# Kernel optimization log

Measured on AMD Instinct MI355X. Metric: run time of the kernel, lower is better.

Reference implementation:

```python
import jax, jax.numpy as jnp
import numpy as np

B = 512       # batch_size
IN = 256      # input_size
H = 512       # hidden_size
OUT = 64      # output_size
N_PAIRS = B - 1   # number of H0 persistence deaths (connected components merges)
TOL = 1e-6    # rtol for torch.isclose
ATOL = 1e-8   # torch default atol
EPS = 0.0     # homology_eps
TARGET_P = 1.0
HOM_P = 1.0
COMP_P = 0.01

_IU = np.triu_indices(B, 1)  # condensed pdist indexing, static


def _mlp(batch, W1, b1, W2, b2, W3, b3, Wout, bout):
    # FeedForward: input->hidden, (n_layers-1) hidden->hidden, hidden->output, ReLU
    h = jax.nn.relu(batch @ W1 + b1)
    h = jax.nn.relu(h @ W2 + b2)
    h = jax.nn.relu(h @ W3 + b3)
    return h @ Wout + bout


def _pdist(y):
    # condensed euclidean pairwise distances, same ordering as torch F.pdist
    d = y[_IU[0]] - y[_IU[1]]                 # [P, OUT]
    return jnp.sqrt(jnp.sum(d * d, axis=-1))  # [P]


def setup_inputs() -> dict:
    key = jax.random.key(0)
    ks = jax.random.split(key, 8)
    batch = jax.random.normal(ks[0], (B, IN), jnp.float32)
    target = jax.random.normal(ks[1], (B, OUT), jnp.float32)
    W1 = jax.random.normal(ks[2], (IN, H), jnp.float32) / np.sqrt(IN)
    W2 = jax.random.normal(ks[3], (H, H), jnp.float32) / np.sqrt(H)
    W3 = jax.random.normal(ks[4], (H, H), jnp.float32) / np.sqrt(H)
    Wout = jax.random.normal(ks[5], (H, OUT), jnp.float32) / np.sqrt(H)
    b1 = jnp.zeros((H,), jnp.float32)
    b2 = jnp.zeros((H,), jnp.float32)
    b3 = jnp.zeros((H,), jnp.float32)
    bout = jnp.zeros((OUT,), jnp.float32)
    # persistence deaths = actual critical pdist values (from the external
    # Vietoris-Rips routine in the original); sample N_PAIRS distinct entries.
    y0 = _mlp(batch, W1, b1, W2, b2, W3, b3, Wout, bout)
    pd0 = np.asarray(_pdist(y0))
    idx = np.random.default_rng(0).choice(pd0.shape[0], N_PAIRS, replace=False)
    persistence_deaths = jnp.asarray(pd0[idx], jnp.float32)
    return {"batch": batch, "target": target,
            "W1": W1, "b1": b1, "W2": W2, "b2": b2, "W3": W3, "b3": b3,
            "Wout": Wout, "bout": bout,
            "persistence_deaths": persistence_deaths}


def reference(batch, target, W1, b1, W2, b2, W3, b3, Wout, bout, persistence_deaths):
    y = _mlp(batch, W1, b1, W2, b2, W3, b3, Wout, bout)   # [B, OUT]
    y_hom = y  # normalize_for_homology = False
    pd = _pdist(y_hom)                                     # [P]
    # vectorized indicator_death over all pairs (replaces per-pair Python loop)
    mask = jnp.any(jnp.isclose(pd[:, None], persistence_deaths[None, :],
                               rtol=TOL, atol=ATOL), axis=1)      # [P] bool
    # homology_dim=0: birth_pdist = 0; norm=1 of selected (death - 0 + eps)
    homology_loss = jnp.sum(jnp.abs(jnp.where(mask, pd + EPS, 0.0)))
    target_loss = jnp.mean((target - y) ** 2)
    compactness_loss = jnp.sum(jnp.abs(y - jnp.mean(y, axis=0, keepdims=True)))
    loss = TARGET_P * target_loss + HOM_P * homology_loss + COMP_P * compactness_loss
    return loss
```

## Files before the change

kernel.cpp:

```cpp
#include <hip/hip_runtime.h>

#define B_    512
#define IN_   256
#define H_    512
#define OUT_  64
#define NDEATH (B_ - 1)
#define NSORT  512
#define RTOL_ 1e-6
#define ATOL_ 1e-8
#define NBLK  256
#define NTHR  512
#define KT    32

typedef __attribute__((ext_vector_type(4))) double d4_t;

__device__ __forceinline__ void ast(double* p, double v) {
    __hip_atomic_store(p, v, __ATOMIC_RELAXED, __HIP_MEMORY_SCOPE_AGENT);
}
__device__ __forceinline__ double ald(const double* p) {
    return __hip_atomic_load(p, __ATOMIC_RELAXED, __HIP_MEMORY_SCOPE_AGENT);
}
__device__ __forceinline__ unsigned aldu(const unsigned* p) {
    return __hip_atomic_load(p, __ATOMIC_RELAXED, __HIP_MEMORY_SCOPE_AGENT);
}
__device__ __forceinline__ void aadd(unsigned* p) {
    __hip_atomic_fetch_add(p, 1u, __ATOMIC_RELAXED, __HIP_MEMORY_SCOPE_AGENT);
}

__device__ __forceinline__ void lbar() {
    asm volatile("s_waitcnt lgkmcnt(0)" ::: "memory");
    __builtin_amdgcn_s_barrier();
    asm volatile("" ::: "memory");
}

__device__ __forceinline__ void gbar(unsigned* cnt, unsigned nb) {
    __syncthreads();
    if (threadIdx.x == 0) {
        aadd(cnt);
        while (aldu(cnt) < nb) __builtin_amdgcn_s_sleep(1);
    }
    __syncthreads();
}

__device__ __forceinline__ void gbar2(unsigned* gslot, unsigned* root,
                                      int leader) {
    __syncthreads();
    if (threadIdx.x == 0) {
        aadd(gslot);
        if (leader) {
            while (aldu(gslot) < 16u) __builtin_amdgcn_s_sleep(1);
            aadd(root);
        }
        while (aldu(root) < 16u) __builtin_amdgcn_s_sleep(1);
    }
    __syncthreads();
}

__device__ void sort_windows(const float* __restrict__ deaths,
                             double* sd, double* slo, double* shi, int t) {
    if (t < NSORT) sd[t] = (t < NDEATH) ? (double)deaths[t] : 1e300;
    __syncthreads();
    for (int k = 2; k <= NSORT; k <<= 1) {
        for (int j = k >> 1; j > 0; j >>= 1) {
            if (t < 256) {
                int l = ((t & ~(j - 1)) << 1) | (t & (j - 1));
                int p = l + j;
                bool up = ((l & k) == 0);
                double a = sd[l], b = sd[p];
                if ((a > b) == up) { sd[l] = b; sd[p] = a; }
            }
            __syncthreads();
        }
    }
    if (t < NSORT) {
        double d = sd[t];
        double w = ATOL_ + RTOL_ * fabs(d);
        slo[t] = d - w;
        shi[t] = d + w;
    }
    __syncthreads();
}

template <typename TIN, bool RELU, int N, int K>
__device__ void gemm_dev(const TIN* __restrict__ A, const float* __restrict__ W,
                         const float* __restrict__ bias, double* __restrict__ C,
                         int tile, int t,
                         double (&As)[2][2][KT][33]) {
    const int lane  = t & 63;
    const int wave4 = (t >> 6) & 3;
    const int w2    = t >> 8;
    const int tg    = t & 255;
    const int wm    = wave4 & 1, wn = wave4 >> 1;
    constexpr int nbx = N >> 5;
    const int row0  = (tile / nbx) << 5;
    const int col0  = (tile % nbx) << 5;

    const int akk   = tg & 31;
    const int amm   = tg >> 5;
    const int kbase = w2 * (K >> 1);
    constexpr int nkt = K >> 6;

    const int mrow  = wm * 16 + (lane & 15);
    const int ncol  = wn * 16 + (lane & 15);
    const int kq    = lane >> 4;

    TIN   ar[3][4];
    float br[3][8];

    auto load_a = [&](int rs, int kt) {
        const int k0 = kbase + (kt << 5);
        #pragma unroll
        for (int p = 0; p < 4; ++p)
            ar[rs][p] = A[(size_t)(row0 + amm + 8 * p) * K + k0 + akk];
    };
    auto load_b = [&](int rs, int kt) {
        const int k0 = kbase + (kt << 5);
        const float* wp = W + (size_t)(k0 + kq) * N + col0 + ncol;
        #pragma unroll
        for (int ks = 0; ks < 8; ++ks)
            br[rs][ks] = wp[(size_t)(4 * ks) * N];
    };
    auto stage_a = [&](int rs, int buf) {
        #pragma unroll
        for (int p = 0; p < 4; ++p)
            As[w2][buf][akk][amm + 8 * p] = (double)ar[rs][p];
    };

    load_a(0, 0); load_b(0, 0);
    if (nkt > 1) { load_a(1, 1); load_b(1, 1); }
    if (nkt > 2) { load_a(2, 2); load_b(2, 2); }
    stage_a(0, 0);
    lbar();

    d4_t c4a = {0.0, 0.0, 0.0, 0.0};
    d4_t c4b = {0.0, 0.0, 0.0, 0.0};

    #pragma unroll
    for (int kt = 0; kt < nkt; ++kt) {
        const int cur = kt & 1;
        const int rs  = kt % 3;
        __builtin_amdgcn_s_setprio(1);
        #pragma unroll
        for (int ks = 0; ks < 4; ++ks) {
            double av = As[w2][cur][ks * 4 + kq][mrow];
            c4a = __builtin_amdgcn_mfma_f64_16x16x4f64(av, (double)br[rs][ks],
                                                       c4a, 0, 0, 0);
        }
        #pragma unroll
        for (int ks = 4; ks < 8; ++ks) {
            double av = As[w2][cur][ks * 4 + kq][mrow];
            c4b = __builtin_amdgcn_mfma_f64_16x16x4f64(av, (double)br[rs][ks],
                                                       c4b, 0, 0, 0);
        }
        __builtin_amdgcn_s_setprio(0);
        if (kt + 3 < nkt) { load_a(rs, kt + 3); load_b(rs, kt + 3); }
        if (kt + 1 < nkt) stage_a((kt + 1) % 3, cur ^ 1);
        lbar();
    }

    d4_t c4 = c4a + c4b;

    double (*cEx)[16][17] = (double (*)[16][17])(&As[0][0][0][0]);
    const int r4 = (lane >> 4) * 4;
    if (w2 == 1) {
        #pragma unroll
        for (int r = 0; r < 4; ++r)
            cEx[wave4][r4 + r][lane & 15] = c4[r];
    }
    lbar();
    if (w2 == 0) {
        #pragma unroll
        for (int r = 0; r < 4; ++r) {
            int row = row0 + wm * 16 + r4 + r;
            int col = col0 + wn * 16 + (lane & 15);
            double v = c4[r] + cEx[wave4][r4 + r][lane & 15] + (double)bias[col];
            if (RELU) v = v > 0.0 ? v : 0.0;
            ast(&C[(size_t)row * N + col], v);
        }
    }
}

__device__ void mc_dev(const float* __restrict__ target,
                       const double* __restrict__ y,
                       double* __restrict__ t_part, double* __restrict__ c_part,
                       int c, int t) {
    const int wave = t >> 6, lane = t & 63;
    double v = y[(size_t)t * OUT_ + c];
    double s = v;
    for (int off = 32; off; off >>= 1) s += __shfl_down(s, off);
    __shared__ double swm[8];
    __shared__ double smean;
    if (lane == 0) swm[wave] = s;
    __syncthreads();
    if (t == 0) {
        double m = 0.0;
        #pragma unroll
        for (int w = 0; w < 8; ++w) m += swm[w];
        smean = m / (double)B_;
    }
    __syncthreads();
    double m = smean;
    double d = (double)target[(size_t)t * OUT_ + c] - v;
    double t_s = d * d;
    double c_s = fabs(v - m);
    for (int off = 32; off; off >>= 1) {
        t_s += __shfl_down(t_s, off);
        c_s += __shfl_down(c_s, off);
    }
    __shared__ double st[8], sc[8];
    if (lane == 0) { st[wave] = t_s; sc[wave] = c_s; }
    __syncthreads();
    if (t == 0) {
        double ts = 0.0, cs = 0.0;
        #pragma unroll
        for (int w = 0; w < 8; ++w) { ts += st[w]; cs += sc[w]; }
        ast(&t_part[c], ts);
        ast(&c_part[c], cs);
    }
}

__device__ __forceinline__ double pair_val(const double* __restrict__ yrow_s,
                                           const double* __restrict__ yj,
                                           const double* __restrict__ slo,
                                           const double* __restrict__ shi) {
    double s = 0.0;
    #pragma unroll
    for (int d = 0; d < OUT_; d += 2) {
        double2 v = *(const double2*)(yj + d);
        double d0 = yrow_s[d]     - v.x;
        double d1 = yrow_s[d + 1] - v.y;
        s = fma(d0, d0, s);
        s = fma(d1, d1, s);
    }
    double pd = sqrt(s);
    int pos = 0;
    #pragma unroll
    for (int step = NSORT / 2; step; step >>= 1) {
        if (slo[pos + step - 1] <= pd) pos += step;
    }
    bool m = (pos > 0) && (shi[pos - 1] >= pd);
    return m ? pd : 0.0;
}

__device__ void pdist_dev(const double* __restrict__ y,
                          double* __restrict__ hom_part, int bid, int t,
                          double* yA, double* yB,
                          const double* slo, const double* shi) {
    const int iA = bid;
    const int iB = 510 - bid;
    if (t < OUT_)            yA[t]        = y[(size_t)iA * OUT_ + t];
    else if (t < 2 * OUT_)   yB[t - OUT_] = y[(size_t)iB * OUT_ + (t - OUT_)];
    __syncthreads();

    double local = 0.0;
    for (int j = iA + 1 + t; j < B_; j += NTHR)
        local += pair_val(yA, y + (size_t)j * OUT_, slo, shi);
    if (iB != iA)
        for (int j = iB + 1 + t; j < B_; j += NTHR)
            local += pair_val(yB, y + (size_t)j * OUT_, slo, shi);

    for (int off = 32; off; off >>= 1) local += __shfl_down(local, off);
    __shared__ double sw[8];
    int wave = t >> 6, lane = t & 63;
    if (lane == 0) sw[wave] = local;
    __syncthreads();
    if (t == 0) {
        double s = 0.0;
        #pragma unroll
        for (int w = 0; w < 8; ++w) s += sw[w];
        ast(&hom_part[bid], s);
    }
}

__global__ __launch_bounds__(NTHR) void fused_k(
    const float* __restrict__ batch, const float* __restrict__ target,
    const float* __restrict__ W1, const float* __restrict__ b1,
    const float* __restrict__ W2, const float* __restrict__ b2,
    const float* __restrict__ W3, const float* __restrict__ b3,
    const float* __restrict__ Wout, const float* __restrict__ bout,
    const float* __restrict__ deaths, float* __restrict__ out,
    double* __restrict__ hA, double* __restrict__ hB,
    double* __restrict__ hC, double* __restrict__ yv,
    double* __restrict__ hom_part, double* __restrict__ t_part,
    double* __restrict__ c_part, unsigned* __restrict__ cnt,
    double* __restrict__ wbc) {
    const int bid = blockIdx.x;
    const int t   = threadIdx.x;
    const int g   = (bid & 7) | ((bid >> 7) << 3);
    const int c   = (bid >> 3) & 15;
    const int tile = g * 16 + c;
    unsigned* gc  = cnt + g * 32;

    __shared__ double As[2][2][KT][33];
    __shared__ double slo[NSORT], shi[NSORT];
    __shared__ double yA[OUT_], yB[OUT_];
    double* sd = &As[0][0][0][0];

    gemm_dev<float,  true, H_, IN_>(batch, W1, b1, hA, tile, t, As);
    gbar(&gc[0], 16);
    gemm_dev<double, true, H_, H_>(hA, W2, b2, hB, tile, t, As);
    gbar(&gc[1], 16);
    gemm_dev<double, true, H_, H_>(hB, W3, b3, hC, tile, t, As);
    gbar(&gc[2], 16);

    if (c < 2) {
        gemm_dev<double, false, OUT_, H_>(hC, Wout, bout, yv, g * 2 + c, t, As);
    } else {
        sort_windows(deaths, sd, slo, shi, t);
        if (g == 0 && c == 2 && t < NSORT) {
            ast(&wbc[t],         slo[t]);
            ast(&wbc[NSORT + t], shi[t]);
        }
    }

    gbar2(&gc[3], &cnt[512], c == 0);
    if (c < 2) {
        if (t < NSORT) {
            slo[t] = ald(&wbc[t]);
            shi[t] = ald(&wbc[NSORT + t]);
        }
        __syncthreads();
    }

    pdist_dev(yv, hom_part, bid, t, yA, yB, slo, shi);
    if (bid < OUT_) mc_dev(target, yv, t_part, c_part, bid, t);

    __syncthreads();
    if (t == 0) {
        aadd(&gc[4]);
        if (c == 0) {
            while (aldu(&gc[4]) < 16u) __builtin_amdgcn_s_sleep(1);
            aadd(&cnt[513]);
        }
    }
    if (bid != 0) return;
    if (t == 0)
        while (aldu(&cnt[513]) < 16u) __builtin_amdgcn_s_sleep(1);
    __syncthreads();

    {
        double h = 0.0, tp = 0.0, cp = 0.0;
        if (t < NBLK) h = ald(&hom_part[t]);
        if (t < OUT_) { tp = ald(&t_part[t]); cp = ald(&c_part[t]); }
        for (int off = 32; off; off >>= 1) {
            h  += __shfl_down(h,  off);
            tp += __shfl_down(tp, off);
            cp += __shfl_down(cp, off);
        }
        __shared__ double sh[8], stp[8], scp[8];
        int wave = t >> 6, lane = t & 63;
        if (lane == 0) { sh[wave] = h; stp[wave] = tp; scp[wave] = cp; }
        __syncthreads();
        if (t == 0) {
            double hs = 0.0, ts = 0.0, cs = 0.0;
            #pragma unroll
            for (int w = 0; w < 8; ++w) {
                hs += sh[w]; ts += stp[w]; cs += scp[w];
            }
            out[0] = (float)(ts / (double)(B_ * OUT_) + hs + 0.01 * cs);
        }
    }
}

extern "C" void kernel_launch(void* const* d_in, const int* in_sizes, int n_in,
                              void* d_out, int out_size, void* d_ws, size_t ws_size,
                              hipStream_t stream) {
    const float* batch  = (const float*)d_in[0];
    const float* target = (const float*)d_in[1];
    const float* W1     = (const float*)d_in[2];
    const float* b1     = (const float*)d_in[3];
    const float* W2     = (const float*)d_in[4];
    const float* b2     = (const float*)d_in[5];
    const float* W3     = (const float*)d_in[6];
    const float* b3     = (const float*)d_in[7];
    const float* Wout   = (const float*)d_in[8];
    const float* bout   = (const float*)d_in[9];
    const float* deaths = (const float*)d_in[10];
    float* out = (float*)d_out;

    double* hA       = (double*)d_ws;
    double* hB       = hA + (size_t)B_ * H_;
    double* hC       = hB + (size_t)B_ * H_;
    double* yv       = hC + (size_t)B_ * H_;
    double* hom_part = yv + (size_t)B_ * OUT_;
    double* t_part   = hom_part + NBLK;
    double* c_part   = t_part + OUT_;
    unsigned* cnt    = (unsigned*)(c_part + OUT_);
    double* wbc      = (double*)(cnt + 576);

    hipMemsetAsync(cnt, 0, 576 * sizeof(unsigned), stream);

    fused_k<<<dim3(NBLK), dim3(NTHR), 0, stream>>>(
        batch, target, W1, b1, W2, b2, W3, b3, Wout, bout, deaths, out,
        hA, hB, hC, yv, hom_part, t_part, c_part, cnt, wbc);
}
```

Measured before the change: 123.4 us.

## Split persistent fused kernel into six launches instead of grid barriers

Replaces the single persistent kernel, which used atomic-counter grid barriers, with separate kernel launches for each MLP layer, the output GEMM, pdist plus the loss partials, and the final reduction. The window sort now runs in an extra block of the first GEMM launch. This drops the spin-wait barriers, the counter memset and the atomic loads and stores, but adds launch overhead between stages and loses the overlap of sorting with the output GEMM.

```diff
diff --git a/kernel.cpp b/kernel.cpp
--- a/kernel.cpp
+++ b/kernel.cpp
@@ -8,52 +8,15 @@
 #define NSORT  512
 #define RTOL_ 1e-6
 #define ATOL_ 1e-8
-#define NBLK  256
 #define NTHR  512
 #define KT    32
 
 typedef __attribute__((ext_vector_type(4))) double d4_t;
-
-__device__ __forceinline__ void ast(double* p, double v) {
-    __hip_atomic_store(p, v, __ATOMIC_RELAXED, __HIP_MEMORY_SCOPE_AGENT);
-}
-__device__ __forceinline__ double ald(const double* p) {
-    return __hip_atomic_load(p, __ATOMIC_RELAXED, __HIP_MEMORY_SCOPE_AGENT);
-}
-__device__ __forceinline__ unsigned aldu(const unsigned* p) {
-    return __hip_atomic_load(p, __ATOMIC_RELAXED, __HIP_MEMORY_SCOPE_AGENT);
-}
-__device__ __forceinline__ void aadd(unsigned* p) {
-    __hip_atomic_fetch_add(p, 1u, __ATOMIC_RELAXED, __HIP_MEMORY_SCOPE_AGENT);
-}
 
 __device__ __forceinline__ void lbar() {
     asm volatile("s_waitcnt lgkmcnt(0)" ::: "memory");
     __builtin_amdgcn_s_barrier();
     asm volatile("" ::: "memory");
-}
-
-__device__ __forceinline__ void gbar(unsigned* cnt, unsigned nb) {
-    __syncthreads();
-    if (threadIdx.x == 0) {
-        aadd(cnt);
-        while (aldu(cnt) < nb) __builtin_amdgcn_s_sleep(1);
-    }
-    __syncthreads();
-}
-
-__device__ __forceinline__ void gbar2(unsigned* gslot, unsigned* root,
-                                      int leader) {
-    __syncthreads();
-    if (threadIdx.x == 0) {
-        aadd(gslot);
-        if (leader) {
-            while (aldu(gslot) < 16u) __builtin_amdgcn_s_sleep(1);
-            aadd(root);
-        }
-        while (aldu(root) < 16u) __builtin_amdgcn_s_sleep(1);
-    }
-    __syncthreads();
 }
 
 __device__ void sort_windows(const float* __restrict__ deaths,
@@ -175,48 +138,52 @@
             int col = col0 + wn * 16 + (lane & 15);
             double v = c4[r] + cEx[wave4][r4 + r][lane & 15] + (double)bias[col];
             if (RELU) v = v > 0.0 ? v : 0.0;
-            ast(&C[(size_t)row * N + col], v);
-        }
-    }
-}
-
-__device__ void mc_dev(const float* __restrict__ target,
-                       const double* __restrict__ y,
-                       double* __restrict__ t_part, double* __restrict__ c_part,
-                       int c, int t) {
-    const int wave = t >> 6, lane = t & 63;
-    double v = y[(size_t)t * OUT_ + c];
-    double s = v;
-    for (int off = 32; off; off >>= 1) s += __shfl_down(s, off);
-    __shared__ double swm[8];
-    __shared__ double smean;
-    if (lane == 0) swm[wave] = s;
-    __syncthreads();
-    if (t == 0) {
-        double m = 0.0;
-        #pragma unroll
-        for (int w = 0; w < 8; ++w) m += swm[w];
-        smean = m / (double)B_;
-    }
-    __syncthreads();
-    double m = smean;
-    double d = (double)target[(size_t)t * OUT_ + c] - v;
-    double t_s = d * d;
-    double c_s = fabs(v - m);
-    for (int off = 32; off; off >>= 1) {
-        t_s += __shfl_down(t_s, off);
-        c_s += __shfl_down(c_s, off);
-    }
-    __shared__ double st[8], sc[8];
-    if (lane == 0) { st[wave] = t_s; sc[wave] = c_s; }
-    __syncthreads();
-    if (t == 0) {
-        double ts = 0.0, cs = 0.0;
-        #pragma unroll
-        for (int w = 0; w < 8; ++w) { ts += st[w]; cs += sc[w]; }
-        ast(&t_part[c], ts);
-        ast(&c_part[c], cs);
-    }
+            C[(size_t)row * N + col] = v;
+        }
+    }
+}
+
+__device__ __forceinline__ int tile_map(int bid) {
+    const int g = (bid & 7) | ((bid >> 7) << 3);
+    const int c = (bid >> 3) & 15;
+    return g * 16 + c;
+}
+
+__global__ __launch_bounds__(NTHR) void g1s_k(
+    const float* __restrict__ batch, const float* __restrict__ W1,
+    const float* __restrict__ b1, double* __restrict__ hA,
+    const float* __restrict__ deaths, double* __restrict__ wbc) {
+    __shared__ double As[2][2][KT][33];
+    const int t = threadIdx.x, bid = blockIdx.x;
+    if (bid == 256) {
+        double* sd  = &As[0][0][0][0];
+        double* slo = sd + NSORT;
+        double* shi = sd + 2 * NSORT;
+        sort_windows(deaths, sd, slo, shi, t);
+        if (t < NSORT) {
+            wbc[t]         = slo[t];
+            wbc[NSORT + t] = shi[t];
+        }
+        return;
+    }
+    gemm_dev<float, true, H_, IN_>(batch, W1, b1, hA, tile_map(bid), t, As);
+}
+
+template <bool RELU>
+__global__ __launch_bounds__(NTHR) void gemm_k(
+    const double* __restrict__ A, const float* __restrict__ W,
+    const float* __restrict__ bias, double* __restrict__ C) {
+    __shared__ double As[2][2][KT][33];
+    gemm_dev<double, RELU, H_, H_>(A, W, bias, C, tile_map(blockIdx.x),
+                                   threadIdx.x, As);
+}
+
+__global__ __launch_bounds__(NTHR) void gout_k(
+    const double* __restrict__ hC, const float* __restrict__ Wout,
+    const float* __restrict__ bout, double* __restrict__ yv) {
+    __shared__ double As[2][2][KT][33];
+    gemm_dev<double, false, OUT_, H_>(hC, Wout, bout, yv, blockIdx.x,
+                                      threadIdx.x, As);
 }
 
 __device__ __forceinline__ double pair_val(const double* __restrict__ yrow_s,
@@ -268,97 +235,83 @@
         double s = 0.0;
         #pragma unroll
         for (int w = 0; w < 8; ++w) s += sw[w];
-        ast(&hom_part[bid], s);
-    }
-}
-
-__global__ __launch_bounds__(NTHR) void fused_k(
-    const float* __restrict__ batch, const float* __restrict__ target,
-    const float* __restrict__ W1, const float* __restrict__ b1,
-    const float* __restrict__ W2, const float* __restrict__ b2,
-    const float* __restrict__ W3, const float* __restrict__ b3,
-    const float* __restrict__ Wout, const float* __restrict__ bout,
-    const float* __restrict__ deaths, float* __restrict__ out,
-    double* __restrict__ hA, double* __restrict__ hB,
-    double* __restrict__ hC, double* __restrict__ yv,
-    double* __restrict__ hom_part, double* __restrict__ t_part,
-    double* __restrict__ c_part, unsigned* __restrict__ cnt,
-    double* __restrict__ wbc) {
-    const int bid = blockIdx.x;
-    const int t   = threadIdx.x;
-    const int g   = (bid & 7) | ((bid >> 7) << 3);
-    const int c   = (bid >> 3) & 15;
-    const int tile = g * 16 + c;
-    unsigned* gc  = cnt + g * 32;
-
-    __shared__ double As[2][2][KT][33];
+        hom_part[bid] = s;
+    }
+}
+
+__device__ void mc_dev(const float* __restrict__ target,
+                       const double* __restrict__ y,
+                       double* __restrict__ t_part, double* __restrict__ c_part,
+                       int c, int t) {
+    const int wave = t >> 6, lane = t & 63;
+    double v = y[(size_t)t * OUT_ + c];
+    double s = v;
+    for (int off = 32; off; off >>= 1) s += __shfl_down(s, off);
+    __shared__ double swm[8];
+    __shared__ double smean;
+    if (lane == 0) swm[wave] = s;
+    __syncthreads();
+    if (t == 0) {
+        double m = 0.0;
+        #pragma unroll
+        for (int w = 0; w < 8; ++w) m += swm[w];
+        smean = m / (double)B_;
+    }
+    __syncthreads();
+    double m = smean;
+    double d = (double)target[(size_t)t * OUT_ + c] - v;
+    double t_s = d * d;
+    double c_s = fabs(v - m);
+    for (int off = 32; off; off >>= 1) {
+        t_s += __shfl_down(t_s, off);
+        c_s += __shfl_down(c_s, off);
+    }
+    __shared__ double st[8], sc[8];
+    if (lane == 0) { st[wave] = t_s; sc[wave] = c_s; }
+    __syncthreads();
+    if (t == 0) {
+        double ts = 0.0, cs = 0.0;
+        #pragma unroll
+        for (int w = 0; w < 8; ++w) { ts += st[w]; cs += sc[w]; }
+        t_part[c] = ts;
+        c_part[c] = cs;
+    }
+}
+
+__global__ __launch_bounds__(NTHR) void pd_k(
+    const double* __restrict__ yv, const float* __restrict__ target,
+    const double* __restrict__ wbc, double* __restrict__ hom_part,
+    double* __restrict__ t_part, double* __restrict__ c_part) {
     __shared__ double slo[NSORT], shi[NSORT];
     __shared__ double yA[OUT_], yB[OUT_];
-    double* sd = &As[0][0][0][0];
-
-    gemm_dev<float,  true, H_, IN_>(batch, W1, b1, hA, tile, t, As);
-    gbar(&gc[0], 16);
-    gemm_dev<double, true, H_, H_>(hA, W2, b2, hB, tile, t, As);
-    gbar(&gc[1], 16);
-    gemm_dev<double, true, H_, H_>(hB, W3, b3, hC, tile, t, As);
-    gbar(&gc[2], 16);
-
-    if (c < 2) {
-        gemm_dev<double, false, OUT_, H_>(hC, Wout, bout, yv, g * 2 + c, t, As);
-    } else {
-        sort_windows(deaths, sd, slo, shi, t);
-        if (g == 0 && c == 2 && t < NSORT) {
-            ast(&wbc[t],         slo[t]);
-            ast(&wbc[NSORT + t], shi[t]);
-        }
-    }
-
-    gbar2(&gc[3], &cnt[512], c == 0);
-    if (c < 2) {
-        if (t < NSORT) {
-            slo[t] = ald(&wbc[t]);
-            shi[t] = ald(&wbc[NSORT + t]);
-        }
-        __syncthreads();
-    }
-
+    const int t = threadIdx.x, bid = blockIdx.x;
+    slo[t] = wbc[t];
+    shi[t] = wbc[NSORT + t];
     pdist_dev(yv, hom_part, bid, t, yA, yB, slo, shi);
     if (bid < OUT_) mc_dev(target, yv, t_part, c_part, bid, t);
-
+}
+
+__global__ __launch_bounds__(NTHR) void fin_k(
+    const double* __restrict__ hom_part, const double* __restrict__ t_part,
+    const double* __restrict__ c_part, float* __restrict__ out) {
+    const int t = threadIdx.x;
+    double h = 0.0, tp = 0.0, cp = 0.0;
+    if (t < 256)  h = hom_part[t];
+    if (t < OUT_) { tp = t_part[t]; cp = c_part[t]; }
+    for (int off = 32; off; off >>= 1) {
+        h  += __shfl_down(h,  off);
+        tp += __shfl_down(tp, off);
+        cp += __shfl_down(cp, off);
+    }
+    __shared__ double sh[8], stp[8], scp[8];
+    int wave = t >> 6, lane = t & 63;
+    if (lane == 0) { sh[wave] = h; stp[wave] = tp; scp[wave] = cp; }
     __syncthreads();
     if (t == 0) {
-        aadd(&gc[4]);
-        if (c == 0) {
-            while (aldu(&gc[4]) < 16u) __builtin_amdgcn_s_sleep(1);
-            aadd(&cnt[513]);
-        }
-    }
-    if (bid != 0) return;
-    if (t == 0)
-        while (aldu(&cnt[513]) < 16u) __builtin_amdgcn_s_sleep(1);
-    __syncthreads();
-
-    {
-        double h = 0.0, tp = 0.0, cp = 0.0;
-        if (t < NBLK) h = ald(&hom_part[t]);
-        if (t < OUT_) { tp = ald(&t_part[t]); cp = ald(&c_part[t]); }
-        for (int off = 32; off; off >>= 1) {
-            h  += __shfl_down(h,  off);
-            tp += __shfl_down(tp, off);
-            cp += __shfl_down(cp, off);
-        }
-        __shared__ double sh[8], stp[8], scp[8];
-        int wave = t >> 6, lane = t & 63;
-        if (lane == 0) { sh[wave] = h; stp[wave] = tp; scp[wave] = cp; }
-        __syncthreads();
-        if (t == 0) {
-            double hs = 0.0, ts = 0.0, cs = 0.0;
-            #pragma unroll
-            for (int w = 0; w < 8; ++w) {
-                hs += sh[w]; ts += stp[w]; cs += scp[w];
-            }
-            out[0] = (float)(ts / (double)(B_ * OUT_) + hs + 0.01 * cs);
-        }
+        double hs = 0.0, ts = 0.0, cs = 0.0;
+        #pragma unroll
+        for (int w = 0; w < 8; ++w) { hs += sh[w]; ts += stp[w]; cs += scp[w]; }
+        out[0] = (float)(ts / (double)(B_ * OUT_) + hs + 0.01 * cs);
     }
 }
 
@@ -383,14 +336,15 @@
     double* hC       = hB + (size_t)B_ * H_;
     double* yv       = hC + (size_t)B_ * H_;
     double* hom_part = yv + (size_t)B_ * OUT_;
-    double* t_part   = hom_part + NBLK;
+    double* t_part   = hom_part + 256;
     double* c_part   = t_part + OUT_;
-    unsigned* cnt    = (unsigned*)(c_part + OUT_);
-    double* wbc      = (double*)(cnt + 576);
-
-    hipMemsetAsync(cnt, 0, 576 * sizeof(unsigned), stream);
-
-    fused_k<<<dim3(NBLK), dim3(NTHR), 0, stream>>>(
-        batch, target, W1, b1, W2, b2, W3, b3, Wout, bout, deaths, out,
-        hA, hB, hC, yv, hom_part, t_part, c_part, cnt, wbc);
-}
+    double* wbc      = c_part + OUT_;
+
+    g1s_k<<<dim3(257), dim3(NTHR), 0, stream>>>(batch, W1, b1, hA, deaths, wbc);
+    gemm_k<true><<<dim3(256), dim3(NTHR), 0, stream>>>(hA, W2, b2, hB);
+    gemm_k<true><<<dim3(256), dim3(NTHR), 0, stream>>>(hB, W3, b3, hC);
+    gout_k<<<dim3(32), dim3(NTHR), 0, stream>>>(hC, Wout, bout, yv);
+    pd_k<<<dim3(256), dim3(NTHR), 0, stream>>>(yv, target, wbc,
+                                               hom_part, t_part, c_part);
+    fin_k<<<dim3(1), dim3(NTHR), 0, stream>>>(hom_part, t_part, c_part, out);
+}
```

Measured after the change: 127.9 us. +3.6%, slower.

## Prefetch next layer's weights before grid barriers and widen A staging to 64-K chunks

Applied to the files above, without the earlier changes.

Each GEMM layer's weight fragments are now loaded into registers before the inter-layer group barrier, so the global weight reads overlap the barrier wait instead of starting after it. The A tile staging is widened from 32 to 64 K per buffer with a two-slot prefetch, which halves the number of LDS sync iterations. The C exchange buffer gets its own shared array. This raises register pressure (a 4x8 float weight array is held across the barriers) and LDS usage (the A staging buffer doubles in size), which may reduce occupancy.

```diff
diff --git a/kernel.cpp b/kernel.cpp
--- a/kernel.cpp
+++ b/kernel.cpp
@@ -10,7 +10,6 @@
 #define ATOL_ 1e-8
 #define NBLK  256
 #define NTHR  512
-#define KT    32
 
 typedef __attribute__((ext_vector_type(4))) double d4_t;
 
@@ -81,11 +80,36 @@
     __syncthreads();
 }
 
+template <int N, int K>
+__device__ __forceinline__ void prefetchB(const float* __restrict__ W,
+                                          int tile, int t, float (&br)[4][8]) {
+    const int lane  = t & 63;
+    const int wave4 = (t >> 6) & 3;
+    const int w2    = t >> 8;
+    const int wn    = wave4 >> 1;
+    constexpr int nbx = N >> 5;
+    const int col0  = (tile % nbx) << 5;
+    const int ncol  = wn * 16 + (lane & 15);
+    const int kq    = lane >> 4;
+    const int kbase = w2 * (K >> 1);
+    constexpr int nch = K >> 6;
+    #pragma unroll
+    for (int s = 0; s < 4; ++s) {
+        if (s < nch) {
+            const int k0 = kbase + (s << 5);
+            const float* wp = W + (size_t)(k0 + kq) * N + col0 + ncol;
+            #pragma unroll
+            for (int ks = 0; ks < 8; ++ks)
+                br[s][ks] = wp[(size_t)(4 * ks) * N];
+        }
+    }
+}
+
 template <typename TIN, bool RELU, int N, int K>
 __device__ void gemm_dev(const TIN* __restrict__ A, const float* __restrict__ W,
                          const float* __restrict__ bias, double* __restrict__ C,
-                         int tile, int t,
-                         double (&As)[2][2][KT][33]) {
+                         int tile, int t, double (&As)[2][2][64][33],
+                         double (&cEx)[4][16][17], float (&br)[4][8]) {
     const int lane  = t & 63;
     const int wave4 = (t >> 6) & 3;
     const int w2    = t >> 8;
@@ -95,40 +119,38 @@
     const int row0  = (tile / nbx) << 5;
     const int col0  = (tile % nbx) << 5;
 
-    const int akk   = tg & 31;
-    const int amm   = tg >> 5;
+    const int akk   = tg & 63;
+    const int amm   = tg >> 6;
     const int kbase = w2 * (K >> 1);
-    constexpr int nkt = K >> 6;
+    constexpr int nbuf = K >> 7;
+    constexpr int nch  = K >> 6;
 
     const int mrow  = wm * 16 + (lane & 15);
     const int ncol  = wn * 16 + (lane & 15);
     const int kq    = lane >> 4;
 
-    TIN   ar[3][4];
-    float br[3][8];
-
-    auto load_a = [&](int rs, int kt) {
-        const int k0 = kbase + (kt << 5);
-        #pragma unroll
-        for (int p = 0; p < 4; ++p)
-            ar[rs][p] = A[(size_t)(row0 + amm + 8 * p) * K + k0 + akk];
+    TIN ar[2][8];
+    auto load_a = [&](int slot, int buf) {
+        const int k0 = kbase + (buf << 6);
+        #pragma unroll
+        for (int p = 0; p < 8; ++p)
+            ar[slot][p] = A[(size_t)(row0 + amm + 4 * p) * K + k0 + akk];
     };
-    auto load_b = [&](int rs, int kt) {
-        const int k0 = kbase + (kt << 5);
+    auto stage_a = [&](int slot, int buf) {
+        #pragma unroll
+        for (int p = 0; p < 8; ++p)
+            As[w2][buf & 1][akk][amm + 4 * p] = (double)ar[slot][p];
+    };
+    auto load_b = [&](int slot, int ch) {
+        const int k0 = kbase + (ch << 5);
         const float* wp = W + (size_t)(k0 + kq) * N + col0 + ncol;
         #pragma unroll
         for (int ks = 0; ks < 8; ++ks)
-            br[rs][ks] = wp[(size_t)(4 * ks) * N];
+            br[slot][ks] = wp[(size_t)(4 * ks) * N];
     };
-    auto stage_a = [&](int rs, int buf) {
-        #pragma unroll
-        for (int p = 0; p < 4; ++p)
-            As[w2][buf][akk][amm + 8 * p] = (double)ar[rs][p];
-    };
-
-    load_a(0, 0); load_b(0, 0);
-    if (nkt > 1) { load_a(1, 1); load_b(1, 1); }
-    if (nkt > 2) { load_a(2, 2); load_b(2, 2); }
+
+    load_a(0, 0);
+    if (nbuf > 1) load_a(1, 1);
     stage_a(0, 0);
     lbar();
 
@@ -136,31 +158,35 @@
     d4_t c4b = {0.0, 0.0, 0.0, 0.0};
 
     #pragma unroll
-    for (int kt = 0; kt < nkt; ++kt) {
-        const int cur = kt & 1;
-        const int rs  = kt % 3;
+    for (int it = 0; it < nbuf; ++it) {
         __builtin_amdgcn_s_setprio(1);
         #pragma unroll
-        for (int ks = 0; ks < 4; ++ks) {
-            double av = As[w2][cur][ks * 4 + kq][mrow];
-            c4a = __builtin_amdgcn_mfma_f64_16x16x4f64(av, (double)br[rs][ks],
-                                                       c4a, 0, 0, 0);
-        }
-        #pragma unroll
-        for (int ks = 4; ks < 8; ++ks) {
-            double av = As[w2][cur][ks * 4 + kq][mrow];
-            c4b = __builtin_amdgcn_mfma_f64_16x16x4f64(av, (double)br[rs][ks],
-                                                       c4b, 0, 0, 0);
+        for (int sub = 0; sub < 2; ++sub) {
+            const int ch = 2 * it + sub;
+            const int bs = ch & 3;
+            #pragma unroll
+            for (int ks = 0; ks < 4; ++ks) {
+                double av = As[w2][it & 1][sub * 32 + ks * 4 + kq][mrow];
+                c4a = __builtin_amdgcn_mfma_f64_16x16x4f64(
+                          av, (double)br[bs][ks], c4a, 0, 0, 0);
+            }
+            #pragma unroll
+            for (int ks = 4; ks < 8; ++ks) {
+                double av = As[w2][it & 1][sub * 32 + ks * 4 + kq][mrow];
+                c4b = __builtin_amdgcn_mfma_f64_16x16x4f64(
+                          av, (double)br[bs][ks], c4b, 0, 0, 0);
+            }
         }
         __builtin_amdgcn_s_setprio(0);
-        if (kt + 3 < nkt) { load_a(rs, kt + 3); load_b(rs, kt + 3); }
-        if (kt + 1 < nkt) stage_a((kt + 1) % 3, cur ^ 1);
+        if (it + 2 < nbuf) load_a(it & 1, it + 2);
+        if (2 * it + 4 < nch) load_b((2 * it + 4) & 3, 2 * it + 4);
+        if (2 * it + 5 < nch) load_b((2 * it + 5) & 3, 2 * it + 5);
+        if (it + 1 < nbuf) stage_a((it + 1) & 1, it + 1);
         lbar();
     }
 
     d4_t c4 = c4a + c4b;
 
-    double (*cEx)[16][17] = (double (*)[16][17])(&As[0][0][0][0]);
     const int r4 = (lane >> 4) * 4;
     if (w2 == 1) {
         #pragma unroll
@@ -291,20 +317,28 @@
     const int tile = g * 16 + c;
     unsigned* gc  = cnt + g * 32;
 
-    __shared__ double As[2][2][KT][33];
+    __shared__ double As[2][2][64][33];
+    __shared__ double cEx[4][16][17];
     __shared__ double slo[NSORT], shi[NSORT];
     __shared__ double yA[OUT_], yB[OUT_];
     double* sd = &As[0][0][0][0];
 
-    gemm_dev<float,  true, H_, IN_>(batch, W1, b1, hA, tile, t, As);
+    float br[4][8];
+
+    prefetchB<H_, IN_>(W1, tile, t, br);
+    gemm_dev<float,  true, H_, IN_>(batch, W1, b1, hA, tile, t, As, cEx, br);
+    prefetchB<H_, H_>(W2, tile, t, br);
     gbar(&gc[0], 16);
-    gemm_dev<double, true, H_, H_>(hA, W2, b2, hB, tile, t, As);
+    gemm_dev<double, true, H_, H_>(hA, W2, b2, hB, tile, t, As, cEx, br);
+    prefetchB<H_, H_>(W3, tile, t, br);
     gbar(&gc[1], 16);
-    gemm_dev<double, true, H_, H_>(hB, W3, b3, hC, tile, t, As);
+    gemm_dev<double, true, H_, H_>(hB, W3, b3, hC, tile, t, As, cEx, br);
+    if (c < 2) prefetchB<OUT_, H_>(Wout, g * 2 + c, t, br);
     gbar(&gc[2], 16);
 
     if (c < 2) {
-        gemm_dev<double, false, OUT_, H_>(hC, Wout, bout, yv, g * 2 + c, t, As);
+        gemm_dev<double, false, OUT_, H_>(hC, Wout, bout, yv, g * 2 + c, t,
+                                          As, cEx, br);
     } else {
         sort_windows(deaths, sd, slo, shi, t);
         if (g == 0 && c == 2 && t < NSORT) {
```

Result: no change. 124.7 us (+1.1%).

## Double block size to 1024 threads with four-way split-K in fused GEMMs

Applied to the files above, without the earlier changes.

Raises threads per block from 512 to 1024 so each GEMM tile splits K four ways instead of two. Each quarter accumulates into four independent MFMA accumulators, and three quarters hand partial sums to a new shared-memory exchange buffer for the first quarter to reduce. The reductions and the mean/compactness code are resized for 16 waves, and threads beyond the batch are masked. This adds parallelism per tile on the serial MLP chain, at the cost of more shared memory and register pressure, a larger reduction, and possibly idle threads in pdist and sort. Parts not shown, such as sort_windows and pdist, may assume 512 threads.

```diff
diff --git a/kernel.cpp b/kernel.cpp
--- a/kernel.cpp
+++ b/kernel.cpp
@@ -9,8 +9,7 @@
 #define RTOL_ 1e-6
 #define ATOL_ 1e-8
 #define NBLK  256
-#define NTHR  512
-#define KT    32
+#define NTHR  1024
 
 typedef __attribute__((ext_vector_type(4))) double d4_t;
 
@@ -84,25 +83,26 @@
 template <typename TIN, bool RELU, int N, int K>
 __device__ void gemm_dev(const TIN* __restrict__ A, const float* __restrict__ W,
                          const float* __restrict__ bias, double* __restrict__ C,
-                         int tile, int t,
-                         double (&As)[2][2][KT][33]) {
-    const int lane  = t & 63;
-    const int wave4 = (t >> 6) & 3;
-    const int w2    = t >> 8;
-    const int tg    = t & 255;
-    const int wm    = wave4 & 1, wn = wave4 >> 1;
+                         int tile, int t, double (&As)[4][2][32][33],
+                         double (&cEx)[3][4][16][17]) {
+    const int lane = t & 63;
+    const int w    = t >> 6;
+    const int quad = w & 3;
+    const int qk   = t >> 8;
+    const int tg   = t & 255;
+    const int wm   = quad & 1, wn = quad >> 1;
     constexpr int nbx = N >> 5;
-    const int row0  = (tile / nbx) << 5;
-    const int col0  = (tile % nbx) << 5;
+    const int row0 = (tile / nbx) << 5;
+    const int col0 = (tile % nbx) << 5;
 
     const int akk   = tg & 31;
     const int amm   = tg >> 5;
-    const int kbase = w2 * (K >> 1);
-    constexpr int nkt = K >> 6;
-
-    const int mrow  = wm * 16 + (lane & 15);
-    const int ncol  = wn * 16 + (lane & 15);
-    const int kq    = lane >> 4;
+    const int kbase = qk * (K >> 2);
+    constexpr int nkt = K >> 7;
+
+    const int mrow = wm * 16 + (lane & 15);
+    const int ncol = wn * 16 + (lane & 15);
+    const int kq   = lane >> 4;
 
     TIN   ar[3][4];
     float br[3][8];
@@ -123,7 +123,7 @@
     auto stage_a = [&](int rs, int buf) {
         #pragma unroll
         for (int p = 0; p < 4; ++p)
-            As[w2][buf][akk][amm + 8 * p] = (double)ar[rs][p];
+            As[qk][buf][akk][amm + 8 * p] = (double)ar[rs][p];
     };
 
     load_a(0, 0); load_b(0, 0);
@@ -134,6 +134,8 @@
 
     d4_t c4a = {0.0, 0.0, 0.0, 0.0};
     d4_t c4b = {0.0, 0.0, 0.0, 0.0};
+    d4_t c4c = {0.0, 0.0, 0.0, 0.0};
+    d4_t c4d = {0.0, 0.0, 0.0, 0.0};
 
     #pragma unroll
     for (int kt = 0; kt < nkt; ++kt) {
@@ -141,16 +143,15 @@
         const int rs  = kt % 3;
         __builtin_amdgcn_s_setprio(1);
         #pragma unroll
-        for (int ks = 0; ks < 4; ++ks) {
-            double av = As[w2][cur][ks * 4 + kq][mrow];
-            c4a = __builtin_amdgcn_mfma_f64_16x16x4f64(av, (double)br[rs][ks],
-                                                       c4a, 0, 0, 0);
-        }
-        #pragma unroll
-        for (int ks = 4; ks < 8; ++ks) {
-            double av = As[w2][cur][ks * 4 + kq][mrow];
-            c4b = __builtin_amdgcn_mfma_f64_16x16x4f64(av, (double)br[rs][ks],
-                                                       c4b, 0, 0, 0);
+        for (int ks = 0; ks < 8; ++ks) {
+            double av = As[qk][cur][ks * 4 + kq][mrow];
+            double bv = (double)br[rs][ks];
+            switch (ks & 3) {
+            case 0: c4a = __builtin_amdgcn_mfma_f64_16x16x4f64(av, bv, c4a, 0, 0, 0); break;
+            case 1: c4b = __builtin_amdgcn_mfma_f64_16x16x4f64(av, bv, c4b, 0, 0, 0); break;
+            case 2: c4c = __builtin_amdgcn_mfma_f64_16x16x4f64(av, bv, c4c, 0, 0, 0); break;
+            default: c4d = __builtin_amdgcn_mfma_f64_16x16x4f64(av, bv, c4d, 0, 0, 0); break;
+            }
         }
         __builtin_amdgcn_s_setprio(0);
         if (kt + 3 < nkt) { load_a(rs, kt + 3); load_b(rs, kt + 3); }
@@ -158,22 +159,24 @@
         lbar();
     }
 
-    d4_t c4 = c4a + c4b;
-
-    double (*cEx)[16][17] = (double (*)[16][17])(&As[0][0][0][0]);
+    d4_t c4 = (c4a + c4b) + (c4c + c4d);
+
     const int r4 = (lane >> 4) * 4;
-    if (w2 == 1) {
+    if (qk >= 1) {
         #pragma unroll
         for (int r = 0; r < 4; ++r)
-            cEx[wave4][r4 + r][lane & 15] = c4[r];
+            cEx[qk - 1][quad][r4 + r][lane & 15] = c4[r];
     }
     lbar();
-    if (w2 == 0) {
+    if (qk == 0) {
         #pragma unroll
         for (int r = 0; r < 4; ++r) {
             int row = row0 + wm * 16 + r4 + r;
             int col = col0 + wn * 16 + (lane & 15);
-            double v = c4[r] + cEx[wave4][r4 + r][lane & 15] + (double)bias[col];
+            double v = c4[r] + cEx[0][quad][r4 + r][lane & 15]
+                             + cEx[1][quad][r4 + r][lane & 15]
+                             + cEx[2][quad][r4 + r][lane & 15]
+                             + (double)bias[col];
             if (RELU) v = v > 0.0 ? v : 0.0;
             ast(&C[(size_t)row * N + col], v);
         }
@@ -185,35 +188,39 @@
                        double* __restrict__ t_part, double* __restrict__ c_part,
                        int c, int t) {
     const int wave = t >> 6, lane = t & 63;
-    double v = y[(size_t)t * OUT_ + c];
+    double v = 0.0;
+    if (t < B_) v = y[(size_t)t * OUT_ + c];
     double s = v;
     for (int off = 32; off; off >>= 1) s += __shfl_down(s, off);
-    __shared__ double swm[8];
+    __shared__ double swm[16];
     __shared__ double smean;
     if (lane == 0) swm[wave] = s;
     __syncthreads();
     if (t == 0) {
         double m = 0.0;
         #pragma unroll
-        for (int w = 0; w < 8; ++w) m += swm[w];
+        for (int w = 0; w < 16; ++w) m += swm[w];
         smean = m / (double)B_;
     }
     __syncthreads();
     double m = smean;
-    double d = (double)target[(size_t)t * OUT_ + c] - v;
-    double t_s = d * d;
-    double c_s = fabs(v - m);
+    double t_s = 0.0, c_s = 0.0;
+    if (t < B_) {
+        double d = (double)target[(size_t)t * OUT_ + c] - v;
+        t_s = d * d;
+        c_s = fabs(v - m);
+    }
     for (int off = 32; off; off >>= 1) {
         t_s += __shfl_down(t_s, off);
         c_s += __shfl_down(c_s, off);
     }
-    __shared__ double st[8], sc[8];
+    __shared__ double st[16], sc[16];
     if (lane == 0) { st[wave] = t_s; sc[wave] = c_s; }
     __syncthreads();
     if (t == 0) {
         double ts = 0.0, cs = 0.0;
         #pragma unroll
-        for (int w = 0; w < 8; ++w) { ts += st[w]; cs += sc[w]; }
+        for (int w = 0; w < 16; ++w) { ts += st[w]; cs += sc[w]; }
         ast(&t_part[c], ts);
         ast(&c_part[c], cs);
     }
@@ -260,14 +267,14 @@
             local += pair_val(yB, y + (size_t)j * OUT_, slo, shi);
 
     for (int off = 32; off; off >>= 1) local += __shfl_down(local, off);
-    __shared__ double sw[8];
+    __shared__ double sw[16];
     int wave = t >> 6, lane = t & 63;
     if (lane == 0) sw[wave] = local;
     __syncthreads();
     if (t == 0) {
         double s = 0.0;
         #pragma unroll
-        for (int w = 0; w < 8; ++w) s += sw[w];
+        for (int w = 0; w < 16; ++w) s += sw[w];
         ast(&hom_part[bid], s);
     }
 }
@@ -291,20 +298,22 @@
     const int tile = g * 16 + c;
     unsigned* gc  = cnt + g * 32;
 
-    __shared__ double As[2][2][KT][33];
+    __shared__ double As[4][2][32][33];
+    __shared__ double cEx[3][4][16][17];
     __shared__ double slo[NSORT], shi[NSORT];
     __shared__ double yA[OUT_], yB[OUT_];
     double* sd = &As[0][0][0][0];
 
-    gemm_dev<float,  true, H_, IN_>(batch, W1, b1, hA, tile, t, As);
+    gemm_dev<float,  true, H_, IN_>(batch, W1, b1, hA, tile, t, As, cEx);
     gbar(&gc[0], 16);
-    gemm_dev<double, true, H_, H_>(hA, W2, b2, hB, tile, t, As);
+    gemm_dev<double, true, H_, H_>(hA, W2, b2, hB, tile, t, As, cEx);
     gbar(&gc[1], 16);
-    gemm_dev<double, true, H_, H_>(hB, W3, b3, hC, tile, t, As);
+    gemm_dev<double, true, H_, H_>(hB, W3, b3, hC, tile, t, As, cEx);
     gbar(&gc[2], 16);
 
     if (c < 2) {
-        gemm_dev<double, false, OUT_, H_>(hC, Wout, bout, yv, g * 2 + c, t, As);
+        gemm_dev<double, false, OUT_, H_>(hC, Wout, bout, yv, g * 2 + c, t,
+                                          As, cEx);
     } else {
         sort_windows(deaths, sd, slo, shi, t);
         if (g == 0 && c == 2 && t < NSORT) {
@@ -347,14 +356,14 @@
             tp += __shfl_down(tp, off);
             cp += __shfl_down(cp, off);
         }
-        __shared__ double sh[8], stp[8], scp[8];
+        __shared__ double sh[16], stp[16], scp[16];
         int wave = t >> 6, lane = t & 63;
         if (lane == 0) { sh[wave] = h; stp[wave] = tp; scp[wave] = cp; }
         __syncthreads();
         if (t == 0) {
             double hs = 0.0, ts = 0.0, cs = 0.0;
             #pragma unroll
-            for (int w = 0; w < 8; ++w) {
+            for (int w = 0; w < 16; ++w) {
                 hs += sh[w]; ts += stp[w]; cs += scp[w];
             }
             out[0] = (float)(ts / (double)(B_ * OUT_) + hs + 0.01 * cs);
```

After: 130.8 us. +6.1%, slower.
